# Optimization experiments

Hardware: AMD Instinct MI355X
Metric: run time of the kernel (lower is better)

## Reference

```python
import jax, jax.numpy as jnp
import numpy as np

GRID_SIZE = 5
SPLINE_ORDER = 3
GRID_RANGE = (-1.0, 1.0)
NUM_BASIS = GRID_SIZE + SPLINE_ORDER  # 8


def setup_inputs() -> dict:
    key = jax.random.key(0)
    k1, k2 = jax.random.split(key)
    x = jax.random.normal(k1, (16, 256, 256, 32), dtype=jnp.float32)
    bound = GRID_RANGE[1] - GRID_RANGE[0]
    grid = jnp.linspace(
        GRID_RANGE[0] - SPLINE_ORDER * bound / GRID_SIZE,
        GRID_RANGE[1] + SPLINE_ORDER * bound / GRID_SIZE,
        GRID_SIZE + 2 * SPLINE_ORDER + 1,
    ).astype(jnp.float32)  # [12], matches tf.linspace(-2.2, 2.2, 12)
    # Per-channel Dense(1, use_bias=False) weights stacked: [in_channel, num_basis]
    W = jax.random.normal(k2, (32, NUM_BASIS), dtype=jnp.float32) * 0.1
    return {"x": x, "grid": grid, "W": W}


def _spline_bases(x, grid, spline_order):
    # Cox-de Boor recursion, basis axis kept last: [..., C, len(grid)-1-order]
    xg = x[..., None]  # [B,H,W,C,1]
    bases = ((xg >= grid[:-1]) & (xg < grid[1:])).astype(x.dtype)  # order-0
    for k in range(1, spline_order + 1):
        left = (xg - grid[:-(k + 1)]) / (grid[k:-1] - grid[:-(k + 1)]) * bases[..., :-1]
        right = (grid[k + 1:] - xg) / (grid[k + 1:] - grid[1:-k]) * bases[..., 1:]
        bases = left + right
    return bases  # [B,H,W,C, grid_size+spline_order]


def reference(x, grid, W):
    bases = _spline_bases(x, grid, SPLINE_ORDER)  # [B,H,W,C,K]
    # Per-channel Dense(1): contract basis axis with channel-specific weights.
    return jnp.einsum('...ck,ck->...c', bases, W)  # [B,H,W,C]
```

## Files before the change

kernel.cpp:

```cpp
#include <hip/hip_runtime.h>


#define FULL_UNROLL _Pragma("unroll")

__device__ __forceinline__ float eval_one(float x, float g0, float inv_h,
                                          const float* __restrict__ P,
                                          const float* __restrict__ Q,
                                          const float* __restrict__ A) {
    float u = (x - g0) * inv_h;
    float d[11];
    FULL_UNROLL
    for (int i = 0; i < 11; ++i) d[i] = u - (float)i;

    float v2p[10];
    v2p[0] = 0.0f;
    FULL_UNROLL
    for (int k = 0; k < 9; ++k) v2p[k + 1] = fmaf(d[k], P[k], Q[k]);

    float acc = 0.0f;
    FULL_UNROLL
    for (int m = 0; m < 10; ++m) {
        float pm1 = (m == 0) ? 0.0f : P[m - 1];
        float vd  = fmaf(d[m], A[m], pm1);
        float v1  = fmaf(d[m], vd, v2p[m]);
        float h   = fmaxf(1.0f - fabsf(d[m + 1]), 0.0f);
        acc = fmaf(h, v1, acc);
    }
    return acc;
}

__global__ void kan_bspline_kernel(const float* __restrict__ x,
                                   const float* __restrict__ grid,
                                   const float* __restrict__ W,
                                   float* __restrict__ out,
                                   int n2) {
    const int tid = blockIdx.x * blockDim.x + threadIdx.x;
    const int c0 = (2 * tid) & 31;

    const float g0 = grid[0];
    const float inv_h = 11.0f / (grid[11] - grid[0]);

    float P[2][9], Q[2][9], A[2][10];
    FULL_UNROLL
    for (int ch = 0; ch < 2; ++ch) {
        const float* wr = W + (c0 + ch) * 8;
        float wpad[12];
        FULL_UNROLL
        for (int j = 0; j < 12; ++j) wpad[j] = 0.0f;
        FULL_UNROLL
        for (int j = 0; j < 8; ++j) wpad[j + 2] = wr[j];
        const float sixth = 1.0f / 6.0f;
        FULL_UNROLL
        for (int k = 0; k < 9; ++k) {
            P[ch][k] = 2.0f * sixth * (wpad[k + 2] - wpad[k + 1]);
            Q[ch][k] = wpad[k + 1];
        }
        FULL_UNROLL
        for (int m = 0; m < 10; ++m) {
            A[ch][m] = sixth * (wpad[m + 2] - 2.0f * wpad[m + 1] + wpad[m]);
        }
    }

    const long long n2l = n2;
    const long long stride = (long long)gridDim.x * blockDim.x;
    const float2* __restrict__ x2 = (const float2*)x;
    float2* __restrict__ o2 = (float2*)out;

    for (long long i = tid; i < n2l; i += stride) {
        float2 xv = x2[i];
        float2 ov;
        ov.x = eval_one(xv.x, g0, inv_h, P[0], Q[0], A[0]);
        ov.y = eval_one(xv.y, g0, inv_h, P[1], Q[1], A[1]);
        o2[i] = ov;
    }
}

extern "C" void kernel_launch(void* const* d_in, const int* in_sizes, int n_in,
                              void* d_out, int out_size, void* d_ws, size_t ws_size,
                              hipStream_t stream) {
    const float* x    = (const float*)d_in[0];
    const float* grid = (const float*)d_in[1];
    const float* W    = (const float*)d_in[2];
    float* out        = (float*)d_out;

    const int n  = in_sizes[0];
    const int n2 = n / 2;

    const int threads = 256;
    const int blocks  = 2048;
    hipLaunchKernelGGL(kan_bspline_kernel, dim3(blocks), dim3(threads), 0, stream,
                       x, grid, W, out, n2);
}
```

Baseline: 245.4 us.

## Replace full B-spline sum with per-interval cubic polynomial lookup in LDS

Precomputes, for each channel and each of the 11 knot intervals, the cubic polynomial coefficients of the weighted spline sum, and stores them in shared memory. Each element then locates its interval with floor, reads one float4 of coefficients and evaluates a Horner cubic, instead of evaluating all ten basis terms. It also widens accesses to float4 with four channels per thread and doubles the block count. The cost is a per-block LDS table build, a barrier, and data-dependent LDS reads that may bank-conflict. The padding by c>>2 is meant to reduce those conflicts.

```diff
diff --git a/kernel.cpp b/kernel.cpp
--- a/kernel.cpp
+++ b/kernel.cpp
@@ -1,93 +1,82 @@
 #include <hip/hip_runtime.h>
 
 
-#define FULL_UNROLL _Pragma("unroll")
+#define NCH 32
+#define NINT 11
 
-__device__ __forceinline__ float eval_one(float x, float g0, float inv_h,
-                                          const float* __restrict__ P,
-                                          const float* __restrict__ Q,
-                                          const float* __restrict__ A) {
-    float u = (x - g0) * inv_h;
-    float d[11];
-    FULL_UNROLL
-    for (int i = 0; i < 11; ++i) d[i] = u - (float)i;
+__global__ __launch_bounds__(256) void kan_bspline_kernel(
+    const float* __restrict__ x,
+    const float* __restrict__ grid,
+    const float* __restrict__ W,
+    float* __restrict__ out,
+    int n4) {
+  __shared__ float4 coef[NCH * NINT + 8];
 
-    float v2p[10];
-    v2p[0] = 0.0f;
-    FULL_UNROLL
-    for (int k = 0; k < 9; ++k) v2p[k + 1] = fmaf(d[k], P[k], Q[k]);
+  const float sixth = 1.0f / 6.0f;
+  for (int e = threadIdx.x; e < NCH * NINT; e += 256) {
+    int c = e / NINT;
+    int i = e - c * NINT;
+    float w[4];
+#pragma unroll
+    for (int k = 0; k < 4; ++k) {
+      int j = i - 3 + k;
+      w[k] = (j >= 0 && j < 8) ? W[c * 8 + j] : 0.0f;
+    }
+    float4 a;
+    a.x = (w[0] + 4.0f * w[1] + w[2]) * sixth;
+    a.y = 0.5f * (w[2] - w[0]);
+    a.z = 0.5f * (w[0] - 2.0f * w[1] + w[2]);
+    a.w = (w[3] - w[0]) * sixth + 0.5f * (w[1] - w[2]);
+    coef[e + (c >> 2)] = a;
+  }
+  __syncthreads();
 
-    float acc = 0.0f;
-    FULL_UNROLL
-    for (int m = 0; m < 10; ++m) {
-        float pm1 = (m == 0) ? 0.0f : P[m - 1];
-        float vd  = fmaf(d[m], A[m], pm1);
-        float v1  = fmaf(d[m], vd, v2p[m]);
-        float h   = fmaxf(1.0f - fabsf(d[m + 1]), 0.0f);
-        acc = fmaf(h, v1, acc);
+  const float g0 = grid[0];
+  const float inv_h = 11.0f / (grid[11] - grid[0]);
+
+  const float4* __restrict__ x4 = (const float4*)x;
+  float4* __restrict__ o4 = (float4*)out;
+
+  const int tid = blockIdx.x * blockDim.x + threadIdx.x;
+  const int stride = gridDim.x * blockDim.x;
+  const int c0 = (4 * tid) & 31;
+  int base[4];
+#pragma unroll
+  for (int k = 0; k < 4; ++k) base[k] = (c0 + k) * NINT + (c0 >> 2);
+
+  for (int idx = tid; idx < n4; idx += stride) {
+    float4 xv = x4[idx];
+    float xs[4] = {xv.x, xv.y, xv.z, xv.w};
+    float rs[4];
+#pragma unroll
+    for (int k = 0; k < 4; ++k) {
+      float u = (xs[k] - g0) * inv_h;
+      float fi = floorf(u);
+      float fic = fminf(fmaxf(fi, 0.0f), 10.0f);
+      float t = u - fic;
+      int i = (int)fic;
+      float4 a = coef[base[k] + i];
+      float r = fmaf(fmaf(fmaf(a.w, t, a.z), t, a.y), t, a.x);
+      rs[k] = (fi >= 0.0f && fi <= 10.0f) ? r : 0.0f;
     }
-    return acc;
-}
-
-__global__ void kan_bspline_kernel(const float* __restrict__ x,
-                                   const float* __restrict__ grid,
-                                   const float* __restrict__ W,
-                                   float* __restrict__ out,
-                                   int n2) {
-    const int tid = blockIdx.x * blockDim.x + threadIdx.x;
-    const int c0 = (2 * tid) & 31;
-
-    const float g0 = grid[0];
-    const float inv_h = 11.0f / (grid[11] - grid[0]);
-
-    float P[2][9], Q[2][9], A[2][10];
-    FULL_UNROLL
-    for (int ch = 0; ch < 2; ++ch) {
-        const float* wr = W + (c0 + ch) * 8;
-        float wpad[12];
-        FULL_UNROLL
-        for (int j = 0; j < 12; ++j) wpad[j] = 0.0f;
-        FULL_UNROLL
-        for (int j = 0; j < 8; ++j) wpad[j + 2] = wr[j];
-        const float sixth = 1.0f / 6.0f;
-        FULL_UNROLL
-        for (int k = 0; k < 9; ++k) {
-            P[ch][k] = 2.0f * sixth * (wpad[k + 2] - wpad[k + 1]);
-            Q[ch][k] = wpad[k + 1];
-        }
-        FULL_UNROLL
-        for (int m = 0; m < 10; ++m) {
-            A[ch][m] = sixth * (wpad[m + 2] - 2.0f * wpad[m + 1] + wpad[m]);
-        }
-    }
-
-    const long long n2l = n2;
-    const long long stride = (long long)gridDim.x * blockDim.x;
-    const float2* __restrict__ x2 = (const float2*)x;
-    float2* __restrict__ o2 = (float2*)out;
-
-    for (long long i = tid; i < n2l; i += stride) {
-        float2 xv = x2[i];
-        float2 ov;
-        ov.x = eval_one(xv.x, g0, inv_h, P[0], Q[0], A[0]);
-        ov.y = eval_one(xv.y, g0, inv_h, P[1], Q[1], A[1]);
-        o2[i] = ov;
-    }
+    float4 ov = make_float4(rs[0], rs[1], rs[2], rs[3]);
+    o4[idx] = ov;
+  }
 }
 
 extern "C" void kernel_launch(void* const* d_in, const int* in_sizes, int n_in,
                               void* d_out, int out_size, void* d_ws, size_t ws_size,
                               hipStream_t stream) {
-    const float* x    = (const float*)d_in[0];
-    const float* grid = (const float*)d_in[1];
-    const float* W    = (const float*)d_in[2];
-    float* out        = (float*)d_out;
+  const float* x    = (const float*)d_in[0];
+  const float* grid = (const float*)d_in[1];
+  const float* W    = (const float*)d_in[2];
+  float* out        = (float*)d_out;
 
-    const int n  = in_sizes[0];
-    const int n2 = n / 2;
+  const int n  = in_sizes[0];
+  const int n4 = n / 4;
 
-    const int threads = 256;
-    const int blocks  = 2048;
-    hipLaunchKernelGGL(kan_bspline_kernel, dim3(blocks), dim3(threads), 0, stream,
-                       x, grid, W, out, n2);
+  const int threads = 256;
+  const int blocks  = 4096;
+  hipLaunchKernelGGL(kan_bspline_kernel, dim3(blocks), dim3(threads), 0, stream,
+                     x, grid, W, out, n4);
 }
```

After: 233.5 us. -4.9%, faster.
